# Kernel tuning notes

Hardware: AMD Instinct MI355X
Metric: run time of the kernel (lower is better)

The kernel has to match this reference:

```python
import jax, jax.numpy as jnp
import numpy as np

B, R, DIM = 4096, 64, 128


def setup_inputs() -> dict:
    key = jax.random.key(0)
    ks = jax.random.split(key, 8)
    return {
        "query_emb": jax.random.normal(ks[0], (B, DIM), jnp.float32),
        "offset_emb": jax.random.normal(ks[1], (B, DIM), jnp.float32),
        "refer_embs": jax.random.normal(ks[2], (B, R, DIM), jnp.float32),
        "query_r": jax.random.normal(ks[3], (B, DIM), jnp.float32),
        "refer_r": jax.random.normal(ks[4], (B, R, DIM), jnp.float32),
        "start_embs": jax.random.normal(ks[5], (B, R, DIM), jnp.float32),
        # attn_layer_1: Linear(2*dim, dim); xavier-uniform-like scale
        "W1": jax.random.uniform(ks[6], (DIM, 2 * DIM), jnp.float32, -0.125, 0.125),
        "b1": jnp.zeros((DIM,), jnp.float32),
        # attn_layer_2: Linear(dim, dim)
        "W2": jax.random.uniform(ks[7], (DIM, DIM), jnp.float32, -0.125, 0.125),
        "b2": jnp.zeros((DIM,), jnp.float32),
    }


def reference(query_emb, offset_emb, refer_embs, query_r, refer_r, start_embs, W1, b1, W2, b2):
    # bias term per neighbor: [B, R, dim]
    bias = refer_embs - (start_embs + refer_r)
    # concat([refer_r, broadcast(query_r)]) @ W1.T split to avoid materializing the concat:
    # W1 = [W1_a | W1_b] over the 2*dim input axis
    W1a, W1b = W1[:, :DIM], W1[:, DIM:]
    h = jnp.einsum('brd,kd->brk', refer_r, W1a) \
        + jnp.einsum('bd,kd->bk', query_r, W1b)[:, None, :] + b1
    h = jax.nn.relu(h)  # [B, R, dim]
    attn = jnp.einsum('brk,dk->brd', h, W2) + b2  # attn_layer_2
    final_refer_emb = jnp.sum(attn * bias, axis=-2)  # [B, dim]
    final_query_emb = query_emb + final_refer_emb
    return (final_query_emb, offset_emb)
```

## Files before the change

### kernel.cpp

```cpp
#include <hip/hip_runtime.h>
#include <hip/hip_bf16.h>
#include <stdint.h>

#define BTOT 4096
#define RR   64
#define DIMD 128

typedef short s16x8 __attribute__((ext_vector_type(8)));
typedef float f32x4 __attribute__((ext_vector_type(4)));

__device__ __forceinline__ unsigned short f2bf(float x) {
  __hip_bfloat16 h = __float2bfloat16(x);
  return __builtin_bit_cast(unsigned short, h);
}
__device__ __forceinline__ unsigned int pk2(float lo, float hi) {
  return ((unsigned int)f2bf(hi) << 16) | (unsigned int)f2bf(lo);
}
__device__ __forceinline__ float bflo(unsigned int u) {
  return __builtin_bit_cast(float, u << 16);
}
__device__ __forceinline__ float bfhi(unsigned int u) {
  return __builtin_bit_cast(float, u & 0xFFFF0000u);
}

__global__ __launch_bounds__(256) void prep_kernel(
    const float* __restrict__ W1, const float* __restrict__ b1,
    const float* __restrict__ query_r, const float* __restrict__ W2,
    const float* __restrict__ offset_emb,
    float* __restrict__ qproj, unsigned short* __restrict__ w1a_t,
    unsigned short* __restrict__ w2_t, float* __restrict__ out)
{
  __shared__ float w1b[128 * 132];
  __shared__ float qrs[256];
  const int tid = threadIdx.x;

  {
    const size_t ob = (size_t)blockIdx.x * 8 * DIMD + (size_t)tid * 4;
    *reinterpret_cast<float4*>(out + (size_t)BTOT * DIMD + ob) =
        *reinterpret_cast<const float4*>(offset_emb + ob);
  }
  {
    const int k = tid >> 1, d0 = (tid & 1) * 64;
    const float* src = W1 + k * 256 + 128 + d0;
    float* dst = &w1b[k * 132 + d0];
    #pragma unroll
    for (int i = 0; i < 64; i += 4)
      *reinterpret_cast<float4*>(dst + i) = *reinterpret_cast<const float4*>(src + i);
  }
  if (blockIdx.x < 2) {
    const float* Wsrc = (blockIdx.x == 0) ? W1 : W2;
    unsigned short* dstw = (blockIdx.x == 0) ? w1a_t : w2_t;
    const int stride = (blockIdx.x == 0) ? 256 : 128;
    for (int i = tid; i < 128 * 128; i += 256) {
      const int k = i >> 7, s = i & 127;
      const int d = 32 * (s >> 5) + 16 * ((s >> 2) & 1) + 4 * ((s >> 3) & 3) + (s & 3);
      dstw[k * 128 + (s ^ ((k & 7) << 3))] = f2bf(Wsrc[k * stride + d]);
    }
  }
  __syncthreads();

  const int b0 = blockIdx.x * 8;
  const int k = tid & 127, bh = tid >> 7;
  for (int p = 0; p < 4; ++p) {
    const int b = b0 + p * 2;
    qrs[tid] = query_r[(size_t)(b + bh) * DIMD + k];
    __syncthreads();
    float acc = b1[k];
    const float* qq = &qrs[bh * 128];
    const float* wr = &w1b[k * 132];
    #pragma unroll
    for (int d = 0; d < 128; d += 4) {
      float4 wv = *reinterpret_cast<const float4*>(wr + d);
      float4 qv = *reinterpret_cast<const float4*>(qq + d);
      acc = fmaf(wv.x, qv.x, acc); acc = fmaf(wv.y, qv.y, acc);
      acc = fmaf(wv.z, qv.z, acc); acc = fmaf(wv.w, qv.w, acc);
    }
    qproj[(size_t)(b + bh) * DIMD + k] = acc;
    __syncthreads();
  }
}

__global__ __launch_bounds__(512) void main_kernel(
    const float* __restrict__ query_emb,
    const float* __restrict__ refer_embs, const float* __restrict__ refer_r,
    const float* __restrict__ start_embs, const float* __restrict__ b2,
    const float* __restrict__ qproj, const unsigned short* __restrict__ w1a_t,
    const unsigned short* __restrict__ w2_t, float* __restrict__ out)
{
  __shared__ unsigned short lds_w1a[128 * 128];
  __shared__ unsigned short lds_w2[128 * 128];

  const int tid  = threadIdx.x;
  const int wave = tid >> 6;
  const int lane = tid & 63;
  const int g    = lane >> 4;
  const int c    = lane & 15;

  {
    const uint4* s1 = reinterpret_cast<const uint4*>(w1a_t);
    const uint4* s2 = reinterpret_cast<const uint4*>(w2_t);
    uint4* d1 = reinterpret_cast<uint4*>(lds_w1a);
    uint4* d2 = reinterpret_cast<uint4*>(lds_w2);
    #pragma unroll
    for (int i = 0; i < 4; ++i) {
      d1[tid + 512 * i] = s1[tid + 512 * i];
      d2[tid + 512 * i] = s2[tid + 512 * i];
    }
  }
  __syncthreads();

  const int swc = (c & 7) << 3;
  const int b = blockIdx.x * 8 + wave;

  f32x4 acc[8];
  #pragma unroll
  for (int nt = 0; nt < 8; ++nt) acc[nt] = (f32x4){0.f, 0.f, 0.f, 0.f};

  union U16x8 { unsigned int u[4]; s16x8 v; };

  for (int it = 0; it < 4; ++it) {
    const size_t rowoff = ((size_t)b * RR + it * 16 + c) * DIMD + 4 * g;
    const float* rp = refer_r    + rowoff;
    const float* ep = refer_embs + rowoff;
    const float* sp = start_embs + rowoff;

    unsigned int bp[16];

    f32x4 Ch[8];
    #pragma unroll
    for (int nt = 0; nt < 8; ++nt)
      Ch[nt] = *reinterpret_cast<const f32x4*>(qproj + (size_t)b * DIMD + 16 * nt + 4 * g);

    #pragma unroll
    for (int ck = 0; ck < 4; ++ck) {
      const float4 rv0 = *reinterpret_cast<const float4*>(rp + 32 * ck);
      const float4 rv1 = *reinterpret_cast<const float4*>(rp + 32 * ck + 16);
      const float4 ev0 = *reinterpret_cast<const float4*>(ep + 32 * ck);
      const float4 ev1 = *reinterpret_cast<const float4*>(ep + 32 * ck + 16);
      const float4 sv0 = *reinterpret_cast<const float4*>(sp + 32 * ck);
      const float4 sv1 = *reinterpret_cast<const float4*>(sp + 32 * ck + 16);
      U16x8 af;
      af.u[0] = pk2(rv0.x, rv0.y); af.u[1] = pk2(rv0.z, rv0.w);
      af.u[2] = pk2(rv1.x, rv1.y); af.u[3] = pk2(rv1.z, rv1.w);
      bp[4 * ck + 0] = pk2(ev0.x - sv0.x - rv0.x, ev0.y - sv0.y - rv0.y);
      bp[4 * ck + 1] = pk2(ev0.z - sv0.z - rv0.z, ev0.w - sv0.w - rv0.w);
      bp[4 * ck + 2] = pk2(ev1.x - sv1.x - rv1.x, ev1.y - sv1.y - rv1.y);
      bp[4 * ck + 3] = pk2(ev1.z - sv1.z - rv1.z, ev1.w - sv1.w - rv1.w);
      #pragma unroll
      for (int nt = 0; nt < 8; ++nt) {
        s16x8 wf = *reinterpret_cast<const s16x8*>(
            &lds_w1a[(nt * 16 + c) * DIMD + ((ck * 32 + g * 8) ^ swc)]);
        Ch[nt] = __builtin_amdgcn_mfma_f32_16x16x32_bf16(wf, af.v, Ch[nt], 0, 0, 0);
      }
      __builtin_amdgcn_sched_barrier(0);
    }

    unsigned int hpk[16];
    #pragma unroll
    for (int nt = 0; nt < 8; ++nt) {
      hpk[2 * nt + 0] = pk2(fmaxf(Ch[nt][0], 0.f), fmaxf(Ch[nt][1], 0.f));
      hpk[2 * nt + 1] = pk2(fmaxf(Ch[nt][2], 0.f), fmaxf(Ch[nt][3], 0.f));
    }

    #pragma unroll
    for (int ntg = 0; ntg < 4; ++ntg) {
      f32x4 Ca0 = *reinterpret_cast<const f32x4*>(b2 + 32 * ntg + 4 * g);
      f32x4 Ca1 = *reinterpret_cast<const f32x4*>(b2 + 32 * ntg + 16 + 4 * g);
      #pragma unroll
      for (int ck = 0; ck < 4; ++ck) {
        U16x8 hf;
        hf.u[0] = hpk[4 * ck + 0]; hf.u[1] = hpk[4 * ck + 1];
        hf.u[2] = hpk[4 * ck + 2]; hf.u[3] = hpk[4 * ck + 3];
        s16x8 w0 = *reinterpret_cast<const s16x8*>(
            &lds_w2[((2 * ntg) * 16 + c) * DIMD + ((ck * 32 + g * 8) ^ swc)]);
        s16x8 w1 = *reinterpret_cast<const s16x8*>(
            &lds_w2[((2 * ntg + 1) * 16 + c) * DIMD + ((ck * 32 + g * 8) ^ swc)]);
        Ca0 = __builtin_amdgcn_mfma_f32_16x16x32_bf16(w0, hf.v, Ca0, 0, 0, 0);
        Ca1 = __builtin_amdgcn_mfma_f32_16x16x32_bf16(w1, hf.v, Ca1, 0, 0, 0);
      }
      acc[2 * ntg][0]     = fmaf(Ca0[0], bflo(bp[4 * ntg + 0]), acc[2 * ntg][0]);
      acc[2 * ntg][1]     = fmaf(Ca0[1], bfhi(bp[4 * ntg + 0]), acc[2 * ntg][1]);
      acc[2 * ntg][2]     = fmaf(Ca0[2], bflo(bp[4 * ntg + 1]), acc[2 * ntg][2]);
      acc[2 * ntg][3]     = fmaf(Ca0[3], bfhi(bp[4 * ntg + 1]), acc[2 * ntg][3]);
      acc[2 * ntg + 1][0] = fmaf(Ca1[0], bflo(bp[4 * ntg + 2]), acc[2 * ntg + 1][0]);
      acc[2 * ntg + 1][1] = fmaf(Ca1[1], bfhi(bp[4 * ntg + 2]), acc[2 * ntg + 1][1]);
      acc[2 * ntg + 1][2] = fmaf(Ca1[2], bflo(bp[4 * ntg + 3]), acc[2 * ntg + 1][2]);
      acc[2 * ntg + 1][3] = fmaf(Ca1[3], bfhi(bp[4 * ntg + 3]), acc[2 * ntg + 1][3]);
    }
    __builtin_amdgcn_sched_barrier(0);
  }

  #pragma unroll
  for (int mask = 1; mask <= 8; mask <<= 1)
    #pragma unroll
    for (int nt = 0; nt < 8; ++nt) {
      acc[nt][0] += __shfl_xor(acc[nt][0], mask);
      acc[nt][1] += __shfl_xor(acc[nt][1], mask);
      acc[nt][2] += __shfl_xor(acc[nt][2], mask);
      acc[nt][3] += __shfl_xor(acc[nt][3], mask);
    }

  if (c == 0) {
    #pragma unroll
    for (int nt = 0; nt < 8; ++nt) {
      const size_t o = (size_t)b * DIMD + 16 * nt + 4 * g;
      const float4 qe = *reinterpret_cast<const float4*>(query_emb + o);
      float4 r;
      r.x = qe.x + acc[nt][0]; r.y = qe.y + acc[nt][1];
      r.z = qe.z + acc[nt][2]; r.w = qe.w + acc[nt][3];
      *reinterpret_cast<float4*>(out + o) = r;
    }
  }
}

extern "C" void kernel_launch(void* const* d_in, const int* in_sizes, int n_in,
                              void* d_out, int out_size, void* d_ws, size_t ws_size,
                              hipStream_t stream) {
  const float* query_emb  = (const float*)d_in[0];
  const float* offset_emb = (const float*)d_in[1];
  const float* refer_embs = (const float*)d_in[2];
  const float* query_r    = (const float*)d_in[3];
  const float* refer_r    = (const float*)d_in[4];
  const float* start_embs = (const float*)d_in[5];
  const float* W1 = (const float*)d_in[6];
  const float* b1 = (const float*)d_in[7];
  const float* W2 = (const float*)d_in[8];
  const float* b2 = (const float*)d_in[9];
  float* out = (float*)d_out;

  float* qproj = (float*)d_ws;
  unsigned short* w1a_t =
      (unsigned short*)((char*)d_ws + (size_t)BTOT * DIMD * sizeof(float));
  unsigned short* w2_t = w1a_t + 128 * 128;

  hipLaunchKernelGGL(prep_kernel, dim3(512), dim3(256), 0, stream,
                     W1, b1, query_r, W2, offset_emb, qproj, w1a_t, w2_t, out);
  hipLaunchKernelGGL(main_kernel, dim3(512), dim3(512), 0, stream,
                     query_emb, refer_embs, refer_r, start_embs,
                     b2, qproj, w1a_t, w2_t, out);
}
```

Measured before the change: 109.0 us.

## Prefetch refer_embs into LDS asynchronously and defer bias computation

refer_embs tiles are now loaded with global_load_lds straight into a per-wave swizzled LDS buffer, one 16-row tile ahead, so the load overlaps the MFMA work of the current tile. The bias is no longer packed to bf16 during the first GEMM. It is computed in fp32 in the epilogue from the LDS data, start_embs loaded one step ahead, and the bf16 refer_r fragments. This lowers register pressure and moves load latency off the critical path. It costs 64KB of extra LDS, which may cut occupancy, and adds explicit waitcnt barriers. Bias precision also changes slightly, because refer_r now enters as bf16.

```diff
diff --git a/kernel.cpp b/kernel.cpp
--- a/kernel.cpp
+++ b/kernel.cpp
@@ -22,6 +22,11 @@
 __device__ __forceinline__ float bfhi(unsigned int u) {
   return __builtin_bit_cast(float, u & 0xFFFF0000u);
 }
+
+#define GLD16(gsrc, ldst)                                                   \
+  __builtin_amdgcn_global_load_lds(                                         \
+      (const __attribute__((address_space(1))) void*)(gsrc),                \
+      (__attribute__((address_space(3))) void*)(ldst), 16, 0, 0)
 
 __global__ __launch_bounds__(256) void prep_kernel(
     const float* __restrict__ W1, const float* __restrict__ b1,
@@ -89,6 +94,7 @@
 {
   __shared__ unsigned short lds_w1a[128 * 128];
   __shared__ unsigned short lds_w2[128 * 128];
+  __shared__ float ebuf[8][16 * 128];
 
   const int tid  = threadIdx.x;
   const int wave = tid >> 6;
@@ -111,6 +117,21 @@
 
   const int swc = (c & 7) << 3;
   const int b = blockIdx.x * 8 + wave;
+  float* myeb = &ebuf[wave][0];
+
+  const int rhalf = lane >> 5;
+  const int jch   = lane & 31;
+
+#define GLOADE(itv) do {                                                      \
+    _Pragma("unroll")                                                         \
+    for (int k_ = 0; k_ < 8; ++k_) {                                          \
+      const int r_  = 2 * k_ + rhalf;                                         \
+      const int ch_ = jch ^ ((r_ & 7) << 1);                                  \
+      const float* gs_ = refer_embs +                                         \
+          ((size_t)b * RR + (itv) * 16 + r_) * DIMD + ch_ * 4;                \
+      GLD16(gs_, myeb + k_ * 256);                                            \
+    }                                                                         \
+  } while (0)
 
   f32x4 acc[8];
   #pragma unroll
@@ -118,39 +139,33 @@
 
   union U16x8 { unsigned int u[4]; s16x8 v; };
 
+  GLOADE(0);
+
   for (int it = 0; it < 4; ++it) {
     const size_t rowoff = ((size_t)b * RR + it * 16 + c) * DIMD + 4 * g;
     const float* rp = refer_r    + rowoff;
-    const float* ep = refer_embs + rowoff;
     const float* sp = start_embs + rowoff;
 
-    unsigned int bp[16];
+    float4 svA = *reinterpret_cast<const float4*>(sp);
+    float4 svB = *reinterpret_cast<const float4*>(sp + 16);
 
     f32x4 Ch[8];
     #pragma unroll
     for (int nt = 0; nt < 8; ++nt)
       Ch[nt] = *reinterpret_cast<const f32x4*>(qproj + (size_t)b * DIMD + 16 * nt + 4 * g);
 
+    U16x8 afq[4];
     #pragma unroll
     for (int ck = 0; ck < 4; ++ck) {
       const float4 rv0 = *reinterpret_cast<const float4*>(rp + 32 * ck);
       const float4 rv1 = *reinterpret_cast<const float4*>(rp + 32 * ck + 16);
-      const float4 ev0 = *reinterpret_cast<const float4*>(ep + 32 * ck);
-      const float4 ev1 = *reinterpret_cast<const float4*>(ep + 32 * ck + 16);
-      const float4 sv0 = *reinterpret_cast<const float4*>(sp + 32 * ck);
-      const float4 sv1 = *reinterpret_cast<const float4*>(sp + 32 * ck + 16);
-      U16x8 af;
-      af.u[0] = pk2(rv0.x, rv0.y); af.u[1] = pk2(rv0.z, rv0.w);
-      af.u[2] = pk2(rv1.x, rv1.y); af.u[3] = pk2(rv1.z, rv1.w);
-      bp[4 * ck + 0] = pk2(ev0.x - sv0.x - rv0.x, ev0.y - sv0.y - rv0.y);
-      bp[4 * ck + 1] = pk2(ev0.z - sv0.z - rv0.z, ev0.w - sv0.w - rv0.w);
-      bp[4 * ck + 2] = pk2(ev1.x - sv1.x - rv1.x, ev1.y - sv1.y - rv1.y);
-      bp[4 * ck + 3] = pk2(ev1.z - sv1.z - rv1.z, ev1.w - sv1.w - rv1.w);
+      afq[ck].u[0] = pk2(rv0.x, rv0.y); afq[ck].u[1] = pk2(rv0.z, rv0.w);
+      afq[ck].u[2] = pk2(rv1.x, rv1.y); afq[ck].u[3] = pk2(rv1.z, rv1.w);
       #pragma unroll
       for (int nt = 0; nt < 8; ++nt) {
         s16x8 wf = *reinterpret_cast<const s16x8*>(
             &lds_w1a[(nt * 16 + c) * DIMD + ((ck * 32 + g * 8) ^ swc)]);
-        Ch[nt] = __builtin_amdgcn_mfma_f32_16x16x32_bf16(wf, af.v, Ch[nt], 0, 0, 0);
+        Ch[nt] = __builtin_amdgcn_mfma_f32_16x16x32_bf16(wf, afq[ck].v, Ch[nt], 0, 0, 0);
       }
       __builtin_amdgcn_sched_barrier(0);
     }
@@ -162,6 +177,10 @@
       hpk[2 * nt + 1] = pk2(fmaxf(Ch[nt][2], 0.f), fmaxf(Ch[nt][3], 0.f));
     }
 
+    asm volatile("s_waitcnt vmcnt(0)" ::: "memory");
+    __builtin_amdgcn_sched_barrier(0);
+
+    const int swz2 = (c & 7) << 1;
     #pragma unroll
     for (int ntg = 0; ntg < 4; ++ntg) {
       f32x4 Ca0 = *reinterpret_cast<const f32x4*>(b2 + 32 * ntg + 4 * g);
@@ -178,17 +197,34 @@
         Ca0 = __builtin_amdgcn_mfma_f32_16x16x32_bf16(w0, hf.v, Ca0, 0, 0, 0);
         Ca1 = __builtin_amdgcn_mfma_f32_16x16x32_bf16(w1, hf.v, Ca1, 0, 0, 0);
       }
-      acc[2 * ntg][0]     = fmaf(Ca0[0], bflo(bp[4 * ntg + 0]), acc[2 * ntg][0]);
-      acc[2 * ntg][1]     = fmaf(Ca0[1], bfhi(bp[4 * ntg + 0]), acc[2 * ntg][1]);
-      acc[2 * ntg][2]     = fmaf(Ca0[2], bflo(bp[4 * ntg + 1]), acc[2 * ntg][2]);
-      acc[2 * ntg][3]     = fmaf(Ca0[3], bfhi(bp[4 * ntg + 1]), acc[2 * ntg][3]);
-      acc[2 * ntg + 1][0] = fmaf(Ca1[0], bflo(bp[4 * ntg + 2]), acc[2 * ntg + 1][0]);
-      acc[2 * ntg + 1][1] = fmaf(Ca1[1], bfhi(bp[4 * ntg + 2]), acc[2 * ntg + 1][1]);
-      acc[2 * ntg + 1][2] = fmaf(Ca1[2], bflo(bp[4 * ntg + 3]), acc[2 * ntg + 1][2]);
-      acc[2 * ntg + 1][3] = fmaf(Ca1[3], bfhi(bp[4 * ntg + 3]), acc[2 * ntg + 1][3]);
-    }
-    __builtin_amdgcn_sched_barrier(0);
-  }
+      float4 svAn, svBn;
+      if (ntg < 3) {
+        svAn = *reinterpret_cast<const float4*>(sp + 32 * (ntg + 1));
+        svBn = *reinterpret_cast<const float4*>(sp + 32 * (ntg + 1) + 16);
+      }
+      const f32x4 ev0 = *reinterpret_cast<const f32x4*>(
+          &myeb[c * 128 + ((8 * ntg + g) ^ swz2) * 4]);
+      const f32x4 ev1 = *reinterpret_cast<const f32x4*>(
+          &myeb[c * 128 + ((8 * ntg + 4 + g) ^ swz2) * 4]);
+      acc[2 * ntg][0] = fmaf(Ca0[0], ev0[0] - svA.x - bflo(afq[ntg].u[0]), acc[2 * ntg][0]);
+      acc[2 * ntg][1] = fmaf(Ca0[1], ev0[1] - svA.y - bfhi(afq[ntg].u[0]), acc[2 * ntg][1]);
+      acc[2 * ntg][2] = fmaf(Ca0[2], ev0[2] - svA.z - bflo(afq[ntg].u[1]), acc[2 * ntg][2]);
+      acc[2 * ntg][3] = fmaf(Ca0[3], ev0[3] - svA.w - bfhi(afq[ntg].u[1]), acc[2 * ntg][3]);
+      acc[2 * ntg + 1][0] = fmaf(Ca1[0], ev1[0] - svB.x - bflo(afq[ntg].u[2]), acc[2 * ntg + 1][0]);
+      acc[2 * ntg + 1][1] = fmaf(Ca1[1], ev1[1] - svB.y - bfhi(afq[ntg].u[2]), acc[2 * ntg + 1][1]);
+      acc[2 * ntg + 1][2] = fmaf(Ca1[2], ev1[2] - svB.z - bflo(afq[ntg].u[3]), acc[2 * ntg + 1][2]);
+      acc[2 * ntg + 1][3] = fmaf(Ca1[3], ev1[3] - svB.w - bfhi(afq[ntg].u[3]), acc[2 * ntg + 1][3]);
+      svA = svAn; svB = svBn;
+      __builtin_amdgcn_sched_barrier(0);
+    }
+
+    if (it < 3) {
+      asm volatile("s_waitcnt lgkmcnt(0)" ::: "memory");
+      __builtin_amdgcn_sched_barrier(0);
+      GLOADE(it + 1);
+    }
+  }
+#undef GLOADE
 
   #pragma unroll
   for (int mask = 1; mask <= 8; mask <<= 1)
```

Result: slower. 305.5 us (+180.3%).

## Move per-wave output accumulators to LDS and cap registers for higher occupancy

Applied to the files above, without the earlier changes.

Replaces the 32-register per-lane accumulator array with a per-wave LDS buffer. Each ntg step now reduces its partial products across the 16 row lanes with xor shuffles, and lane c==0 adds the result into LDS. Launch bounds now request 4 blocks per CU so the compiler limits register use. The trade is many more shuffle reductions, four per output group per iteration instead of one final reduction, plus extra LDS traffic. LDS use (64KB of weights per block) may itself limit how many blocks fit on a CU.

```diff
diff --git a/kernel.cpp b/kernel.cpp
--- a/kernel.cpp
+++ b/kernel.cpp
@@ -80,7 +80,7 @@
   }
 }
 
-__global__ __launch_bounds__(512) void main_kernel(
+__global__ __launch_bounds__(512, 4) void main_kernel(
     const float* __restrict__ query_emb,
     const float* __restrict__ refer_embs, const float* __restrict__ refer_r,
     const float* __restrict__ start_embs, const float* __restrict__ b2,
@@ -89,6 +89,7 @@
 {
   __shared__ unsigned short lds_w1a[128 * 128];
   __shared__ unsigned short lds_w2[128 * 128];
+  __shared__ float accw[8][128];
 
   const int tid  = threadIdx.x;
   const int wave = tid >> 6;
@@ -111,10 +112,10 @@
 
   const int swc = (c & 7) << 3;
   const int b = blockIdx.x * 8 + wave;
-
-  f32x4 acc[8];
-  #pragma unroll
-  for (int nt = 0; nt < 8; ++nt) acc[nt] = (f32x4){0.f, 0.f, 0.f, 0.f};
+  float* myacc = accw[wave];
+
+  myacc[lane] = 0.f;
+  myacc[lane + 64] = 0.f;
 
   union U16x8 { unsigned int u[4]; s16x8 v; };
 
@@ -178,36 +179,43 @@
         Ca0 = __builtin_amdgcn_mfma_f32_16x16x32_bf16(w0, hf.v, Ca0, 0, 0, 0);
         Ca1 = __builtin_amdgcn_mfma_f32_16x16x32_bf16(w1, hf.v, Ca1, 0, 0, 0);
       }
-      acc[2 * ntg][0]     = fmaf(Ca0[0], bflo(bp[4 * ntg + 0]), acc[2 * ntg][0]);
-      acc[2 * ntg][1]     = fmaf(Ca0[1], bfhi(bp[4 * ntg + 0]), acc[2 * ntg][1]);
-      acc[2 * ntg][2]     = fmaf(Ca0[2], bflo(bp[4 * ntg + 1]), acc[2 * ntg][2]);
-      acc[2 * ntg][3]     = fmaf(Ca0[3], bfhi(bp[4 * ntg + 1]), acc[2 * ntg][3]);
-      acc[2 * ntg + 1][0] = fmaf(Ca1[0], bflo(bp[4 * ntg + 2]), acc[2 * ntg + 1][0]);
-      acc[2 * ntg + 1][1] = fmaf(Ca1[1], bfhi(bp[4 * ntg + 2]), acc[2 * ntg + 1][1]);
-      acc[2 * ntg + 1][2] = fmaf(Ca1[2], bflo(bp[4 * ntg + 3]), acc[2 * ntg + 1][2]);
-      acc[2 * ntg + 1][3] = fmaf(Ca1[3], bfhi(bp[4 * ntg + 3]), acc[2 * ntg + 1][3]);
-    }
-    __builtin_amdgcn_sched_barrier(0);
-  }
-
-  #pragma unroll
-  for (int mask = 1; mask <= 8; mask <<= 1)
-    #pragma unroll
-    for (int nt = 0; nt < 8; ++nt) {
-      acc[nt][0] += __shfl_xor(acc[nt][0], mask);
-      acc[nt][1] += __shfl_xor(acc[nt][1], mask);
-      acc[nt][2] += __shfl_xor(acc[nt][2], mask);
-      acc[nt][3] += __shfl_xor(acc[nt][3], mask);
-    }
+      float s[8];
+      s[0] = Ca0[0] * bflo(bp[4 * ntg + 0]);
+      s[1] = Ca0[1] * bfhi(bp[4 * ntg + 0]);
+      s[2] = Ca0[2] * bflo(bp[4 * ntg + 1]);
+      s[3] = Ca0[3] * bfhi(bp[4 * ntg + 1]);
+      s[4] = Ca1[0] * bflo(bp[4 * ntg + 2]);
+      s[5] = Ca1[1] * bfhi(bp[4 * ntg + 2]);
+      s[6] = Ca1[2] * bflo(bp[4 * ntg + 3]);
+      s[7] = Ca1[3] * bfhi(bp[4 * ntg + 3]);
+      #pragma unroll
+      for (int j = 0; j < 8; ++j) {
+        s[j] += __shfl_xor(s[j], 1);
+        s[j] += __shfl_xor(s[j], 2);
+        s[j] += __shfl_xor(s[j], 4);
+        s[j] += __shfl_xor(s[j], 8);
+      }
+      if (c == 0) {
+        f32x4* a0 = reinterpret_cast<f32x4*>(&myacc[16 * (2 * ntg) + 4 * g]);
+        f32x4* a1 = reinterpret_cast<f32x4*>(&myacc[16 * (2 * ntg + 1) + 4 * g]);
+        f32x4 v0 = *a0, v1 = *a1;
+        v0[0] += s[0]; v0[1] += s[1]; v0[2] += s[2]; v0[3] += s[3];
+        v1[0] += s[4]; v1[1] += s[5]; v1[2] += s[6]; v1[3] += s[7];
+        *a0 = v0; *a1 = v1;
+      }
+      __builtin_amdgcn_sched_barrier(0);
+    }
+  }
 
   if (c == 0) {
     #pragma unroll
     for (int nt = 0; nt < 8; ++nt) {
       const size_t o = (size_t)b * DIMD + 16 * nt + 4 * g;
       const float4 qe = *reinterpret_cast<const float4*>(query_emb + o);
+      const f32x4 a = *reinterpret_cast<const f32x4*>(&myacc[16 * nt + 4 * g]);
       float4 r;
-      r.x = qe.x + acc[nt][0]; r.y = qe.y + acc[nt][1];
-      r.z = qe.z + acc[nt][2]; r.w = qe.w + acc[nt][3];
+      r.x = qe.x + a[0]; r.y = qe.y + a[1];
+      r.z = qe.z + a[2]; r.w = qe.w + a[3];
       *reinterpret_cast<float4*>(out + o) = r;
     }
   }
```

New measurement: 179.9 us. 65.1% more time.
